# Performance work log

Measured on AMD Instinct MI355X. Metric: run time of the kernel, lower is better.

The kernel has to match this reference:

```python
import jax, jax.numpy as jnp
import numpy as np

N = 50000          # num nodes
E = 800000         # num edges (avg degree 16)
D_IN = 128         # input_size
H = 128            # hidden_size
BN_EPS = 1e-5


def setup_inputs() -> dict:
    key = jax.random.key(0)
    ks = jax.random.split(key, 16)
    std = 1.0 / np.sqrt(H)
    u = lambda k, shape: jax.random.uniform(k, shape, jnp.float32, -std, std)
    return {
        "x": jax.random.normal(ks[0], (N, D_IN), jnp.float32),
        "hx": jax.random.normal(ks[1], (N, H), jnp.float32),
        "cx": jax.random.normal(ks[2], (N, H), jnp.float32),
        "edge_src": jax.random.randint(ks[3], (E,), 0, N, jnp.int32),
        "edge_dst": jax.random.randint(ks[4], (E,), 0, N, jnp.int32),
        "edge_weight": jax.random.uniform(ks[5], (E,), jnp.float32) / 16.0,  # ~normalized adj values
        "gcn_weight": u(ks[6], (D_IN, H)),
        "bias": u(ks[7], (H,)),
        "x2h_w": u(ks[8], (4 * H, H)),
        "x2h_b": u(ks[9], (4 * H,)),
        "h2h_w": u(ks[10], (4 * H, H)),
        "h2h_b": u(ks[11], (4 * H,)),
        "bn_gamma": u(ks[12], (H,)),
        "bn_beta": u(ks[13], (H,)),
        "bn_mean": jnp.zeros((H,), jnp.float32),
        "bn_var": jnp.ones((H,), jnp.float32),
    }


def reference(x, hx, cx, edge_src, edge_dst, edge_weight, gcn_weight, bias,
              x2h_w, x2h_b, h2h_w, h2h_b, bn_gamma, bn_beta, bn_mean, bn_var):
    # GCN: support = x @ W, then sparse adj @ support via gather/segment-sum
    support = x @ gcn_weight                                   # (N, H)
    msgs = edge_weight[:, None] * support[edge_src]            # (E, H)
    agg = jax.ops.segment_sum(msgs, edge_dst, num_segments=N)  # (N, H) = spmm(adj, support)
    h = jax.nn.relu(agg)
    # dropout: eval mode -> identity
    h = h + bias
    # BatchNorm1d (eval mode, running stats)
    h = (h - bn_mean) * jax.lax.rsqrt(bn_var + BN_EPS) * bn_gamma + bn_beta
    # fused LSTM gates: x2h(h) + h2h(hx)
    gates = h @ x2h_w.T + x2h_b + hx @ h2h_w.T + h2h_b         # (N, 4H)
    i_g, f_g, g_g, o_g = jnp.split(gates, 4, axis=1)
    cy = cx * jax.nn.sigmoid(f_g) + jax.nn.sigmoid(i_g) * jnp.tanh(g_g)
    hy = jax.nn.sigmoid(o_g) * jnp.tanh(cy)
    return hy, cy
```

## Files before the change

### kernel.cpp

```cpp
#include <hip/hip_runtime.h>

#define NN 50000
#define NE 800000
#define HH 128
#define BN_EPS 1e-5f
#define SCAN_NB ((NN + 255) / 256)

typedef unsigned short u16;
typedef unsigned int u32;
typedef short bf16x8 __attribute__((ext_vector_type(8)));
typedef float f32x4 __attribute__((ext_vector_type(4)));

static __device__ __forceinline__ float bf2f(u16 u){
  union { u32 i; float f; } v; v.i = ((u32)u) << 16; return v.f;
}
static __device__ __forceinline__ u16 f2bf(float f){
  union { float f; u32 i; } v; v.f = f;
  u32 x = v.i;
  return (u16)((x + 0x7fffu + ((x >> 16) & 1u)) >> 16);
}
static __device__ __forceinline__ float sigm(float x){
  return 1.f / (1.f + __expf(-x));
}
static __device__ __forceinline__ float tanh_fast(float x){
  return 1.f - 2.f / (1.f + __expf(2.f * x));
}


__global__ void zero_kernel(int* __restrict__ p, int n){
  int i = blockIdx.x * blockDim.x + threadIdx.x;
  if (i < n) p[i] = 0;
}

__global__ void hist_kernel(const int* __restrict__ dst, int* __restrict__ counts, int E){
  int e = blockIdx.x * blockDim.x + threadIdx.x;
  if (e < E) atomicAdd(&counts[dst[e]], 1);
}


__global__ __launch_bounds__(256) void scan_bsum(
    const int* __restrict__ counts, int* __restrict__ bsums, int n){
  int i = blockIdx.x * 256 + threadIdx.x;
  int v = (i < n) ? counts[i] : 0;
#pragma unroll
  for (int off = 1; off < 64; off <<= 1) v += __shfl_xor(v, off);
  __shared__ int ws[4];
  if ((threadIdx.x & 63) == 0) ws[threadIdx.x >> 6] = v;
  __syncthreads();
  if (threadIdx.x == 0) bsums[blockIdx.x] = ws[0] + ws[1] + ws[2] + ws[3];
}

__global__ __launch_bounds__(256) void scan_tops(int* __restrict__ bsums, int nb){
  __shared__ int sh[256];
  int t = threadIdx.x;
  int v = (t < nb) ? bsums[t] : 0;
  sh[t] = v;
  __syncthreads();
  for (int off = 1; off < 256; off <<= 1){
    int u = (t >= off) ? sh[t - off] : 0;
    __syncthreads();
    sh[t] += u;
    __syncthreads();
  }
  if (t < nb) bsums[t] = sh[t] - v;
}

__global__ __launch_bounds__(256) void scan_final(
    const int* __restrict__ counts, const int* __restrict__ bsums,
    int* __restrict__ offs, int* __restrict__ cursor, int n){
  __shared__ int sh[256];
  int t = threadIdx.x;
  int i = blockIdx.x * 256 + t;
  int v = (i < n) ? counts[i] : 0;
  sh[t] = v;
  __syncthreads();
  for (int off = 1; off < 256; off <<= 1){
    int u = (t >= off) ? sh[t - off] : 0;
    __syncthreads();
    sh[t] += u;
    __syncthreads();
  }
  int excl = sh[t] - v + bsums[blockIdx.x];
  if (i < n){ offs[i] = excl; cursor[i] = excl; }
}

__global__ void scatter_kernel(const int* __restrict__ src, const int* __restrict__ dst,
                               const float* __restrict__ w, int* __restrict__ cursor,
                               int2* __restrict__ esw, int E){
  int e = blockIdx.x * blockDim.x + threadIdx.x;
  if (e < E){
    int d = dst[e];
    int pos = atomicAdd(&cursor[d], 1);
    esw[pos] = make_int2(src[e], __float_as_int(w[e]));
  }
}


__global__ void prep_pack(const float* __restrict__ x2hw, const float* __restrict__ h2hw,
                          const float* __restrict__ x2hb, const float* __restrict__ h2hb,
                          const float* __restrict__ gcnw,
                          u16* __restrict__ wcat, u16* __restrict__ wgcn,
                          float* __restrict__ bsum){
  int i = blockIdx.x * blockDim.x + threadIdx.x;
  int n = i >> 8, k = i & 255;
  float v = (k < 128) ? x2hw[n * 128 + k] : h2hw[n * 128 + (k - 128)];
  wcat[i] = f2bf(v);
  if (i < 16384){
    int nn = i >> 7, kk = i & 127;
    wgcn[i] = f2bf(gcnw[kk * 128 + nn]);
  }
  if (i < 512) bsum[i] = x2hb[i] + h2hb[i];
}

__global__ __launch_bounds__(256) void support_mfma(
    const float* __restrict__ x, const u16* __restrict__ wgcn,
    u16* __restrict__ support, int N){
  int tid = threadIdx.x;
  int wave = tid >> 6, lane = tid & 63;
  int c = lane & 15, q = lane >> 4;
  int row0 = blockIdx.x * 64 + wave * 16;
  int arow = row0 + c; if (arow > N - 1) arow = N - 1;
  f32x4 acc[8];
#pragma unroll
  for (int t = 0; t < 8; t++) acc[t] = (f32x4){0.f, 0.f, 0.f, 0.f};

  const u16* wp = wgcn + (size_t)c * 128 + q * 8;
#pragma unroll
  for (int k0 = 0; k0 < 128; k0 += 32){
    const float* ap = x + (size_t)arow * 128 + k0 + q * 8;
    float4 f0 = *(const float4*)ap;
    float4 f1 = *(const float4*)(ap + 4);
    u16 tmp[8] = {f2bf(f0.x), f2bf(f0.y), f2bf(f0.z), f2bf(f0.w),
                  f2bf(f1.x), f2bf(f1.y), f2bf(f1.z), f2bf(f1.w)};
    bf16x8 afrag = *(bf16x8*)tmp;
#pragma unroll
    for (int t = 0; t < 8; t++){
      bf16x8 bfrag = *(const bf16x8*)(wp + (size_t)t * 16 * 128 + k0);
      acc[t] = __builtin_amdgcn_mfma_f32_16x16x32_bf16(afrag, bfrag, acc[t], 0, 0, 0);
    }
  }
#pragma unroll
  for (int t = 0; t < 8; t++){
#pragma unroll
    for (int j = 0; j < 4; j++){
      int r = row0 + q * 4 + j;
      if (r < N) support[(size_t)r * 128 + t * 16 + c] = f2bf(acc[t][j]);
    }
  }
}

__global__ __launch_bounds__(256) void agg_bn2(
    const u16* __restrict__ support, const int2* __restrict__ esw,
    const int* __restrict__ offs, const int* __restrict__ counts,
    const float* __restrict__ bias, const float* __restrict__ gamma,
    const float* __restrict__ beta, const float* __restrict__ mean,
    const float* __restrict__ var, const float* __restrict__ hx,
    u16* __restrict__ hbn, u16* __restrict__ hxb, int N){
  int wid = blockIdx.x * 4 + (threadIdx.x >> 6);
  int lane = threadIdx.x & 63;
  if (wid >= N) return;
  int c = lane * 2;
  float2 hv = *(const float2*)(hx + (size_t)wid * HH + c);
  int start = offs[wid];
  int deg   = counts[wid];
  float a0 = 0.f, a1 = 0.f;
  for (int base = 0; base < deg; base += 64){
    int cnt = deg - base; if (cnt > 64) cnt = 64;
    int2 my = make_int2(0, 0);
    if (lane < cnt) my = esw[start + base + lane];
    int e = 0;
    for (; e + 8 <= cnt; e += 8){
      int s[8]; float g[8]; u32 u[8];
#pragma unroll
      for (int k = 0; k < 8; k++){
        s[k] = __shfl(my.x, e + k);
        g[k] = __int_as_float(__shfl(my.y, e + k));
      }
#pragma unroll
      for (int k = 0; k < 8; k++)
        u[k] = *(const u32*)(support + (size_t)s[k] * HH + c);
#pragma unroll
      for (int k = 0; k < 8; k++){
        a0 = fmaf(g[k], bf2f((u16)(u[k] & 0xffffu)), a0);
        a1 = fmaf(g[k], bf2f((u16)(u[k] >> 16)), a1);
      }
    }
    for (; e + 4 <= cnt; e += 4){
      int s[4]; float g[4]; u32 u[4];
#pragma unroll
      for (int k = 0; k < 4; k++){
        s[k] = __shfl(my.x, e + k);
        g[k] = __int_as_float(__shfl(my.y, e + k));
      }
#pragma unroll
      for (int k = 0; k < 4; k++)
        u[k] = *(const u32*)(support + (size_t)s[k] * HH + c);
#pragma unroll
      for (int k = 0; k < 4; k++){
        a0 = fmaf(g[k], bf2f((u16)(u[k] & 0xffffu)), a0);
        a1 = fmaf(g[k], bf2f((u16)(u[k] >> 16)), a1);
      }
    }
    for (; e < cnt; e++){
      int   si = __shfl(my.x, e);
      float gi = __int_as_float(__shfl(my.y, e));
      u32 ui = *(const u32*)(support + (size_t)si * HH + c);
      a0 = fmaf(gi, bf2f((u16)(ui & 0xffffu)), a0);
      a1 = fmaf(gi, bf2f((u16)(ui >> 16)), a1);
    }
  }
  float h0 = fmaxf(a0, 0.f) + bias[c];
  float h1 = fmaxf(a1, 0.f) + bias[c + 1];
  float s0 = gamma[c]     * rsqrtf(var[c]     + BN_EPS);
  float s1 = gamma[c + 1] * rsqrtf(var[c + 1] + BN_EPS);
  float r0 = (h0 - mean[c])     * s0 + beta[c];
  float r1 = (h1 - mean[c + 1]) * s1 + beta[c + 1];
  u32 pack = (u32)f2bf(r0) | ((u32)f2bf(r1) << 16);
  *(u32*)(hbn + (size_t)wid * HH + c) = pack;
  u32 hp = (u32)f2bf(hv.x) | ((u32)f2bf(hv.y) << 16);
  *(u32*)(hxb + (size_t)wid * HH + c) = hp;
}

__global__ __launch_bounds__(256, 2) void gates_mfma2(
    const u16* __restrict__ hbn, const u16* __restrict__ hxb,
    const u16* __restrict__ wcat, const float* __restrict__ bsum,
    const float* __restrict__ cx, float* __restrict__ out, int N){
  int tid = threadIdx.x;
  int wave = tid >> 6, lane = tid & 63;
  int c = lane & 15, q = lane >> 4;
  int half = blockIdx.y;
  int hloc = half * 64 + wave * 16 + c;

  bf16x8 btile[4][8];
#pragma unroll
  for (int g = 0; g < 4; g++){
    int ntile = g * 8 + half * 4 + wave;
    const u16* bp = wcat + (size_t)(ntile * 16 + c) * 256 + q * 8;
#pragma unroll
    for (int kk = 0; kk < 8; kk++)
      btile[g][kk] = *(const bf16x8*)(bp + kk * 32);
  }
  float bi  = bsum[hloc];
  float bf_ = bsum[128 + hloc];
  float bg  = bsum[256 + hloc];
  float bo  = bsum[384 + hloc];
  const size_t NH = (size_t)N * HH;

  const int nchunk = (N + 63) >> 6;
  for (int chunk = blockIdx.x; chunk < nchunk; chunk += gridDim.x){
    int row0 = chunk * 64;
    f32x4 acc[4][4];
#pragma unroll
    for (int b = 0; b < 4; b++)
#pragma unroll
      for (int g = 0; g < 4; g++) acc[b][g] = (f32x4){0.f, 0.f, 0.f, 0.f};
    int ar[4];
#pragma unroll
    for (int b = 0; b < 4; b++){
      int r = row0 + b * 16 + c; if (r > N - 1) r = N - 1;
      ar[b] = r;
    }
#pragma unroll
    for (int kk = 0; kk < 8; kk++){
      const u16* base = (kk < 4) ? (hbn + (size_t)(kk * 32) + q * 8)
                                 : (hxb + (size_t)((kk - 4) * 32) + q * 8);
#pragma unroll
      for (int b = 0; b < 4; b++){
        bf16x8 a = *(const bf16x8*)(base + (size_t)ar[b] * 128);
#pragma unroll
        for (int g = 0; g < 4; g++)
          acc[b][g] = __builtin_amdgcn_mfma_f32_16x16x32_bf16(a, btile[g][kk], acc[b][g], 0, 0, 0);
      }
    }
#pragma unroll
    for (int b = 0; b < 4; b++){
#pragma unroll
      for (int j = 0; j < 4; j++){
        int r = row0 + b * 16 + q * 4 + j;
        if (r < N){
          float gi = acc[b][0][j] + bi;
          float gf = acc[b][1][j] + bf_;
          float gg = acc[b][2][j] + bg;
          float go = acc[b][3][j] + bo;
          float is = sigm(gi), fs = sigm(gf), gt = tanh_fast(gg), os = sigm(go);
          float co = cx[(size_t)r * HH + hloc];
          float cyv = co * fs + is * gt;
          out[(size_t)r * HH + hloc]      = os * tanh_fast(cyv);
          out[NH + (size_t)r * HH + hloc] = cyv;
        }
      }
    }
  }
}


extern "C" void kernel_launch(void* const* d_in, const int* in_sizes, int n_in,
                              void* d_out, int out_size, void* d_ws, size_t ws_size,
                              hipStream_t stream){
  const float* x     = (const float*)d_in[0];
  const float* hx    = (const float*)d_in[1];
  const float* cx    = (const float*)d_in[2];
  const int*   esrc  = (const int*)d_in[3];
  const int*   edst  = (const int*)d_in[4];
  const float* ew    = (const float*)d_in[5];
  const float* gcn_w = (const float*)d_in[6];
  const float* bias  = (const float*)d_in[7];
  const float* x2hw  = (const float*)d_in[8];
  const float* x2hb  = (const float*)d_in[9];
  const float* h2hw  = (const float*)d_in[10];
  const float* h2hb  = (const float*)d_in[11];
  const float* bn_g  = (const float*)d_in[12];
  const float* bn_b  = (const float*)d_in[13];
  const float* bn_m  = (const float*)d_in[14];
  const float* bn_v  = (const float*)d_in[15];
  float* out = (float*)d_out;

  char* w = (char*)d_ws;
  u16* support = (u16*)w; w += (((size_t)NN * HH * 2) + 255) & ~(size_t)255;
  u16* hbn     = (u16*)w; w += (((size_t)NN * HH * 2) + 255) & ~(size_t)255;
  u16* hxb     = (u16*)w; w += (((size_t)NN * HH * 2) + 255) & ~(size_t)255;
  int* counts  = (int*)w; w += (((size_t)NN * 4) + 255) & ~(size_t)255;
  int* offs    = (int*)w; w += (((size_t)NN * 4) + 255) & ~(size_t)255;
  int* cursor  = (int*)w; w += (((size_t)NN * 4) + 255) & ~(size_t)255;
  int* bsums   = (int*)w; w += (((size_t)SCAN_NB * 4) + 255) & ~(size_t)255;
  int2* esw    = (int2*)w; w += (((size_t)NE * 8) + 255) & ~(size_t)255;
  u16* wcat    = (u16*)w; w += (((size_t)512 * 256 * 2) + 255) & ~(size_t)255;
  u16* wgcn    = (u16*)w; w += (((size_t)128 * 128 * 2) + 255) & ~(size_t)255;
  float* bsum  = (float*)w; w += (((size_t)512 * 4) + 255) & ~(size_t)255;

  prep_pack<<<512, 256, 0, stream>>>(x2hw, h2hw, x2hb, h2hb, gcn_w, wcat, wgcn, bsum);
  zero_kernel<<<(NN + 255) / 256, 256, 0, stream>>>(counts, NN);
  hist_kernel<<<(NE + 255) / 256, 256, 0, stream>>>(edst, counts, NE);
  scan_bsum<<<SCAN_NB, 256, 0, stream>>>(counts, bsums, NN);
  scan_tops<<<1, 256, 0, stream>>>(bsums, SCAN_NB);
  scan_final<<<SCAN_NB, 256, 0, stream>>>(counts, bsums, offs, cursor, NN);
  scatter_kernel<<<(NE + 255) / 256, 256, 0, stream>>>(esrc, edst, ew, cursor, esw, NE);
  support_mfma<<<(NN + 63) / 64, 256, 0, stream>>>(x, wgcn, support, NN);
  agg_bn2<<<(NN + 3) / 4, 256, 0, stream>>>(support, esw, offs, counts,
                                            bias, bn_g, bn_b, bn_m, bn_v, hx, hbn, hxb, NN);
  gates_mfma2<<<dim3((NN + 63) / 64, 2), 256, 0, stream>>>(hbn, hxb, wcat, bsum, cx, out, NN);
}
```

Measured before the change: 367.2 us.

## Stage gate weights in LDS and retile gates kernel over 16-column hidden groups

The gates kernel now loads each block's weight slice (16 hidden columns across 4 gates, K=256) into shared memory once, instead of holding 32 bf16x8 weight fragments per lane in registers. Each wave handles 32 rows rather than 64, and the grid becomes a fixed 128x8 persistent layout with 8 hidden groups. The goal is lower register pressure and higher occupancy (launch bounds 4). The trade-off is that every activation row is now read by 8 column-group blocks instead of 2, which raises global and L2 traffic, and each MFMA pair needs an extra LDS read.

```diff
diff --git a/kernel.cpp b/kernel.cpp
--- a/kernel.cpp
+++ b/kernel.cpp
@@ -221,62 +221,63 @@
   *(u32*)(hxb + (size_t)wid * HH + c) = hp;
 }
 
-__global__ __launch_bounds__(256, 2) void gates_mfma2(
+__global__ __launch_bounds__(256, 4) void gates_mfma3(
     const u16* __restrict__ hbn, const u16* __restrict__ hxb,
     const u16* __restrict__ wcat, const float* __restrict__ bsum,
     const float* __restrict__ cx, float* __restrict__ out, int N){
+  __shared__ bf16x8 lds_b[2048];
   int tid = threadIdx.x;
   int wave = tid >> 6, lane = tid & 63;
   int c = lane & 15, q = lane >> 4;
-  int half = blockIdx.y;
-  int hloc = half * 64 + wave * 16 + c;
-
-  bf16x8 btile[4][8];
-#pragma unroll
-  for (int g = 0; g < 4; g++){
-    int ntile = g * 8 + half * 4 + wave;
-    const u16* bp = wcat + (size_t)(ntile * 16 + c) * 256 + q * 8;
-#pragma unroll
-    for (int kk = 0; kk < 8; kk++)
-      btile[g][kk] = *(const bf16x8*)(bp + kk * 32);
-  }
+  int hg = blockIdx.y;
+  int hloc = hg * 16 + c;
+
+#pragma unroll
+  for (int i = 0; i < 8; i++){
+    int idx = i * 256 + tid;
+    int f = idx >> 6, l = idx & 63;
+    int g = f >> 3, kk = f & 7;
+    int lq = l >> 4, lc = l & 15;
+    const u16* src = wcat + (size_t)(g * 128 + hg * 16 + lc) * 256 + kk * 32 + lq * 8;
+    lds_b[idx] = *(const bf16x8*)src;
+  }
+  __syncthreads();
+
   float bi  = bsum[hloc];
   float bf_ = bsum[128 + hloc];
   float bg  = bsum[256 + hloc];
   float bo  = bsum[384 + hloc];
   const size_t NH = (size_t)N * HH;
 
-  const int nchunk = (N + 63) >> 6;
+  const int nchunk = (N + 127) >> 7;
   for (int chunk = blockIdx.x; chunk < nchunk; chunk += gridDim.x){
-    int row0 = chunk * 64;
-    f32x4 acc[4][4];
-#pragma unroll
-    for (int b = 0; b < 4; b++)
+    int rowbase = chunk * 128 + wave * 32;
+    f32x4 acc[2][4];
+#pragma unroll
+    for (int b = 0; b < 2; b++)
 #pragma unroll
       for (int g = 0; g < 4; g++) acc[b][g] = (f32x4){0.f, 0.f, 0.f, 0.f};
-    int ar[4];
-#pragma unroll
-    for (int b = 0; b < 4; b++){
-      int r = row0 + b * 16 + c; if (r > N - 1) r = N - 1;
-      ar[b] = r;
-    }
+    int ar0 = rowbase + c;      if (ar0 > N - 1) ar0 = N - 1;
+    int ar1 = rowbase + 16 + c; if (ar1 > N - 1) ar1 = N - 1;
+
 #pragma unroll
     for (int kk = 0; kk < 8; kk++){
-      const u16* base = (kk < 4) ? (hbn + (size_t)(kk * 32) + q * 8)
-                                 : (hxb + (size_t)((kk - 4) * 32) + q * 8);
-#pragma unroll
-      for (int b = 0; b < 4; b++){
-        bf16x8 a = *(const bf16x8*)(base + (size_t)ar[b] * 128);
-#pragma unroll
-        for (int g = 0; g < 4; g++)
-          acc[b][g] = __builtin_amdgcn_mfma_f32_16x16x32_bf16(a, btile[g][kk], acc[b][g], 0, 0, 0);
-      }
-    }
-#pragma unroll
-    for (int b = 0; b < 4; b++){
+      const u16* abase = ((kk < 4) ? (hbn + (size_t)(kk * 32))
+                                   : (hxb + (size_t)((kk - 4) * 32))) + q * 8;
+      bf16x8 a0 = *(const bf16x8*)(abase + (size_t)ar0 * 128);
+      bf16x8 a1 = *(const bf16x8*)(abase + (size_t)ar1 * 128);
+#pragma unroll
+      for (int g = 0; g < 4; g++){
+        bf16x8 bfrag = lds_b[(g * 8 + kk) * 64 + lane];
+        acc[0][g] = __builtin_amdgcn_mfma_f32_16x16x32_bf16(a0, bfrag, acc[0][g], 0, 0, 0);
+        acc[1][g] = __builtin_amdgcn_mfma_f32_16x16x32_bf16(a1, bfrag, acc[1][g], 0, 0, 0);
+      }
+    }
+#pragma unroll
+    for (int b = 0; b < 2; b++){
 #pragma unroll
       for (int j = 0; j < 4; j++){
-        int r = row0 + b * 16 + q * 4 + j;
+        int r = rowbase + b * 16 + q * 4 + j;
         if (r < N){
           float gi = acc[b][0][j] + bi;
           float gf = acc[b][1][j] + bf_;
@@ -338,5 +339,5 @@
   support_mfma<<<(NN + 63) / 64, 256, 0, stream>>>(x, wgcn, support, NN);
   agg_bn2<<<(NN + 3) / 4, 256, 0, stream>>>(support, esw, offs, counts,
                                             bias, bn_g, bn_b, bn_m, bn_v, hx, hbn, hxb, NN);
-  gates_mfma2<<<dim3((NN + 63) / 64, 2), 256, 0, stream>>>(hbn, hxb, wcat, bsum, cx, out, NN);
-}
+  gates_mfma3<<<dim3(128, 8), 256, 0, stream>>>(hbn, hxb, wcat, bsum, cx, out, NN);
+}
```

New measurement: 408.8 us. +11.3%, slower.
